# Performance work log

Hardware: AMD Instinct MI355X
Metric: run time of the kernel (lower is better)

Reference implementation:

```python
import jax, jax.numpy as jnp
import numpy as np

DIM = 256
DEPTH = 6
HEADS = 8
DH = DIM // HEADS            # 32
BUCKET = 64
TEMP = 0.75                  # sort-net softmax temperature
FF = 4 * DIM
B, T = 4, 8192


def layernorm(x, g, b, eps=1e-5):
    m = x.mean(-1, keepdims=True)
    v = ((x - m) ** 2).mean(-1, keepdims=True)
    return (x - m) * jax.lax.rsqrt(v + eps) * g + b


def sinkhorn_attn(q, k, v):
    # q,k,v: (bh, t, dh). Bucketed attention with differentiable top-1 bucket routing
    bh, t, dh = q.shape
    nb = t // BUCKET
    bq = q.reshape(bh, nb, BUCKET, dh)
    bk = k.reshape(bh, nb, BUCKET, dh)
    bv = v.reshape(bh, nb, BUCKET, dh)
    # sort net: bucket summaries -> routing matrix R (differentiable_topk, k=1)
    sq = bq.mean(2)                                   # (bh, nb, dh)
    sk = bk.mean(2)
    R = jnp.einsum('bie,bje->bij', sq, sk) * (dh ** -0.5)
    probs = jax.nn.softmax(R / TEMP, axis=-1)
    top = jnp.max(probs, axis=-1, keepdims=True)      # (bh, nb, 1)
    idx = jnp.argmax(probs, axis=-1)                  # (bh, nb)
    Rtop = jax.nn.one_hot(idx, nb, dtype=q.dtype) * top
    # gather routed key/value buckets (weighted by routing prob)
    bk_r = jnp.einsum('bij,bjtd->bitd', Rtop, bk)
    bv_r = jnp.einsum('bij,bjtd->bitd', Rtop, bv)
    K = jnp.concatenate([bk_r, bk], axis=2)           # (bh, nb, 2*BUCKET, dh)
    V = jnp.concatenate([bv_r, bv], axis=2)
    dots = jnp.einsum('buie,buje->buij', bq, K) * (dh ** -0.5)
    attn = jax.nn.softmax(dots, axis=-1)
    out = jnp.einsum('buij,buje->buie', attn, V)
    return out.reshape(bh, t, dh)


def setup_inputs() -> dict:
    key = jax.random.key(0)
    ks = jax.random.split(key, 18)
    s = 0.02
    f32 = jnp.float32
    inp = {
        'x': jax.random.normal(ks[0], (B, DIM, T), f32),
        'pe0': jax.random.normal(ks[1], (T // BUCKET, DIM), f32) * s,
        'pe1': jax.random.normal(ks[2], (BUCKET, DIM), f32) * s,
        'ln1_g': jnp.ones((DEPTH, DIM), f32),
        'ln1_b': jnp.zeros((DEPTH, DIM), f32),
        'Wq': jax.random.normal(ks[3], (DEPTH, DIM, DIM), f32) * s,
        'Wkv': jax.random.normal(ks[4], (DEPTH, DIM, 2 * DIM), f32) * s,
        'Wo': jax.random.normal(ks[5], (DEPTH, DIM, DIM), f32) * s,
        'bo': jnp.zeros((DEPTH, DIM), f32),
        'ln2_g': jnp.ones((DEPTH, DIM), f32),
        'ln2_b': jnp.zeros((DEPTH, DIM), f32),
        'W1': jax.random.normal(ks[6], (DEPTH, DIM, FF), f32) * s,
        'b1': jnp.zeros((DEPTH, FF), f32),
        'W2': jax.random.normal(ks[7], (DEPTH, FF, DIM), f32) * s,
        'b2': jnp.zeros((DEPTH, DIM), f32),
        'gf': jnp.ones((DIM,), f32),
        'bf': jnp.zeros((DIM,), f32),
    }
    return inp


def _forward(x, pe0, pe1, ln1_g, ln1_b, Wq, Wkv, Wo, bo, ln2_g, ln2_b, W1, b1, W2, b2, gf, bf):
    b, _, t = x.shape
    y = jnp.transpose(x, (0, 2, 1))                      # (b, t, dim)
    pos = (pe0[:, None, :] + pe1[None, :, :]).reshape(-1, DIM)[:t]
    y = y + pos

    def split_heads(u):
        return u.reshape(b, t, HEADS, DH).transpose(0, 2, 1, 3).reshape(b * HEADS, t, DH)

    def step(y, p):
        g1, b1_, wq, wkv, wo, bo_, g2, b2_, w1, bb1, w2, bb2 = p
        h = layernorm(y, g1, b1_)
        q = h @ wq
        k, v = jnp.split(h @ wkv, 2, axis=-1)
        o = sinkhorn_attn(split_heads(q), split_heads(k), split_heads(v))
        o = o.reshape(b, HEADS, t, DH).transpose(0, 2, 1, 3).reshape(b, t, DIM)
        y = y + o @ wo + bo_
        h = layernorm(y, g2, b2_)
        y = y + jax.nn.gelu(h @ w1 + bb1, approximate=False) @ w2 + bb2
        return y, None

    y, _ = jax.lax.scan(step, y, (ln1_g, ln1_b, Wq, Wkv, Wo, bo, ln2_g, ln2_b, W1, b1, W2, b2))
    y = layernorm(y, gf, bf)
    return jnp.transpose(y, (0, 2, 1))


def reference(x, pe0, pe1, ln1_g, ln1_b, Wq, Wkv, Wo, bo, ln2_g, ln2_b, W1, b1, W2, b2, gf, bf):
    return _forward(x, pe0, pe1, ln1_g, ln1_b, Wq, Wkv, Wo, bo, ln2_g, ln2_b, W1, b1, W2, b2, gf, bf)
```

## Files before the change

### kernel.cpp

```cpp
#include <hip/hip_runtime.h>
#include <cstdint>
#include <cstddef>

#define T_LEN 8192
#define DIMC  256
#define NBUCK 128
#define BHEAD 32
#define MROWS 32768

typedef __attribute__((ext_vector_type(8))) short bf16x8;
typedef __attribute__((ext_vector_type(4))) float f32x4;

__device__ __forceinline__ ushort f2bf(float x) {
  union { float f; unsigned u; } v; v.f = x;
  unsigned r = v.u + 0x7fffu + ((v.u >> 16) & 1u);
  return (ushort)(r >> 16);
}
__device__ __forceinline__ float bf2f(ushort u) {
  union { unsigned u; float f; } v; v.u = ((unsigned)u) << 16; return v.f;
}

__device__ __forceinline__ void gld16(const void* g, void* l) {
  __builtin_amdgcn_global_load_lds((const __attribute__((address_space(1))) void*)g,
                                   (__attribute__((address_space(3))) void*)l, 16, 0, 0);
}

__device__ __forceinline__ float fast_gelu(float v) {
  float t2 = fmaf(v * v, 0.07135481283f, 1.5957691216f);
  float z  = v * t2;
  float e  = __expf(-z);
  return v * __builtin_amdgcn_rcpf(1.0f + e);
}

__global__ __launch_bounds__(256)
void add_pos_k(const float* __restrict__ x, const float* __restrict__ pe0,
               const float* __restrict__ pe1, float* __restrict__ y) {
  __shared__ float tile[32][33];
  int b  = blockIdx.z;
  int t0 = blockIdx.x * 32;
  int d0 = blockIdx.y * 32;
  int tj = threadIdx.x;
  int di = threadIdx.y;
#pragma unroll
  for (int k = 0; k < 4; k++) {
    int d = d0 + di + k * 8;
    tile[di + k * 8][tj] = x[((size_t)b * DIMC + d) * T_LEN + t0 + tj];
  }
  __syncthreads();
#pragma unroll
  for (int k = 0; k < 4; k++) {
    int t = t0 + di + k * 8;
    int d = d0 + tj;
    y[((size_t)b * T_LEN + t) * DIMC + d] =
        tile[tj][di + k * 8] + pe0[(size_t)(t >> 6) * DIMC + d] + pe1[(size_t)(t & 63) * DIMC + d];
  }
}

__global__ __launch_bounds__(256)
void layernorm_k(const float* __restrict__ x, const float* __restrict__ g,
                 const float* __restrict__ b, ushort* __restrict__ o) {
  int row  = blockIdx.x * 4 + (threadIdx.x >> 6);
  int lane = threadIdx.x & 63;
  const float4* xr = (const float4*)(x + (size_t)row * DIMC);
  float4 v = xr[lane];
  float s  = v.x + v.y + v.z + v.w;
  float s2 = v.x * v.x + v.y * v.y + v.z * v.z + v.w * v.w;
#pragma unroll
  for (int off = 32; off; off >>= 1) {
    s  += __shfl_xor(s, off);
    s2 += __shfl_xor(s2, off);
  }
  float mean = s * (1.0f / 256.0f);
  float var  = s2 * (1.0f / 256.0f) - mean * mean;
  float r    = rsqrtf(var + 1e-5f);
  float4 gv = ((const float4*)g)[lane];
  float4 bv = ((const float4*)b)[lane];
  ushort4 o4;
  o4.x = f2bf((v.x - mean) * r * gv.x + bv.x);
  o4.y = f2bf((v.y - mean) * r * gv.y + bv.y);
  o4.z = f2bf((v.z - mean) * r * gv.z + bv.z);
  o4.w = f2bf((v.w - mean) * r * gv.w + bv.w);
  ((ushort4*)(o + (size_t)row * DIMC))[lane] = o4;
}

__global__ __launch_bounds__(256)
void wt_bf16_k(const float* __restrict__ W, ushort* __restrict__ Wt,
               int K, int N, size_t outStride) {
  __shared__ float t[32][33];
  int l = blockIdx.z;
  const float* Wl = W + (size_t)l * K * N;
  ushort* Wtl = Wt + (size_t)l * outStride;
  int n0 = blockIdx.x * 32, k0 = blockIdx.y * 32;
  int tx = threadIdx.x, ty = threadIdx.y;
#pragma unroll
  for (int p = 0; p < 4; p++)
    t[ty + p * 8][tx] = Wl[(size_t)(k0 + ty + p * 8) * N + n0 + tx];
  __syncthreads();
#pragma unroll
  for (int p = 0; p < 4; p++)
    Wtl[(size_t)(n0 + ty + p * 8) * K + k0 + tx] = f2bf(t[tx][ty + p * 8]);
}

template <int EPI>
__global__ __launch_bounds__(256)
void gemm_bf16(const ushort* __restrict__ A, const ushort* __restrict__ Bt,
               const float* __restrict__ bias, ushort* __restrict__ Cbf,
               int N, int K, int lda, int ldb) {
  __shared__ ushort As[128 * 32];
  __shared__ ushort Bs[128 * 32];
  __shared__ ushort eb[4][16][66];
  int tid = threadIdx.x;
  int w = tid >> 6, lane = tid & 63;
  int bm = blockIdx.x << 7, bn = blockIdx.y << 7;
  int wm = (w >> 1) << 6, wn = (w & 1) << 6;
  int l15 = lane & 15, quad = lane >> 4;

  int off0 = (w << 11) + (lane << 4);
  int off1 = off0 + 1024;
  int r0 = off0 >> 6;
  int r1 = off1 >> 6;
  int swc = (((lane & 3) ^ ((lane >> 3) & 3)) << 3);
  const ushort* ga0 = A + (size_t)(bm + r0) * lda + swc;
  const ushort* ga1 = A + (size_t)(bm + r1) * lda + swc;
  const ushort* gb0 = Bt + (size_t)(bn + r0) * ldb + swc;
  const ushort* gb1 = Bt + (size_t)(bn + r1) * ldb + swc;
  ushort* lA0 = As + (w << 10);
  ushort* lA1 = lA0 + 512;
  ushort* lB0 = Bs + (w << 10);
  ushort* lB1 = lB0 + 512;

  int sq = quad ^ ((l15 >> 1) & 3);

  f32x4 acc[4][4];
#pragma unroll
  for (int i = 0; i < 4; i++)
#pragma unroll
    for (int j = 0; j < 4; j++) {
      f32x4 z = {0.f, 0.f, 0.f, 0.f};
      acc[i][j] = z;
    }

  for (int k0 = 0; k0 < K; k0 += 32) {
    gld16(ga0 + k0, lA0);
    gld16(ga1 + k0, lA1);
    gld16(gb0 + k0, lB0);
    gld16(gb1 + k0, lB1);
    __syncthreads();
    bf16x8 aF[4], bF[4];
#pragma unroll
    for (int i = 0; i < 4; i++)
      aF[i] = *(const bf16x8*)(As + ((wm + (i << 4) + l15) << 5) + (sq << 3));
#pragma unroll
    for (int j = 0; j < 4; j++)
      bF[j] = *(const bf16x8*)(Bs + ((wn + (j << 4) + l15) << 5) + (sq << 3));
#pragma unroll
    for (int i = 0; i < 4; i++)
#pragma unroll
      for (int j = 0; j < 4; j++)
        acc[i][j] = __builtin_amdgcn_mfma_f32_16x16x32_bf16(aF[i], bF[j], acc[i][j], 0, 0, 0);
    __syncthreads();
  }

  float bvj[4];
  if (EPI == 1) {
#pragma unroll
    for (int j = 0; j < 4; j++) bvj[j] = bias[bn + wn + (j << 4) + l15];
  }
#pragma unroll
  for (int i = 0; i < 4; i++) {
#pragma unroll
    for (int j = 0; j < 4; j++) {
#pragma unroll
      for (int r = 0; r < 4; r++) {
        float v = acc[i][j][r];
        if (EPI == 1) v = fast_gelu(v + bvj[j]);
        eb[w][(quad << 2) + r][(j << 4) + l15] = f2bf(v);
      }
    }
#pragma unroll
    for (int h = 0; h < 2; h++) {
      int chunk = (h << 6) + lane;
      int row = chunk >> 3, c8 = (chunk & 7) << 3;
      bf16x8 vv = *(const bf16x8*)&eb[w][row][c8];
      *(bf16x8*)&Cbf[(size_t)(bm + wm + (i << 4) + row) * N + bn + wn + c8] = vv;
    }
  }
}

template <int FINAL>
__global__ __launch_bounds__(256)
void oproj_ln_k(const ushort* __restrict__ A, const ushort* __restrict__ Bt,
                const float* __restrict__ bias, float* __restrict__ y,
                const float* __restrict__ g, const float* __restrict__ b,
                ushort* __restrict__ obf, int K, int lda) {
  __shared__ ushort smem[64 * 264];
  __shared__ float red[2][64][2];
  __shared__ float stat[64][2];
  ushort* As = smem;
  ushort* Bs = smem + 2048;
  int tid = threadIdx.x;
  int wid = tid >> 6, lane = tid & 63;
  int l15 = lane & 15, quad = lane >> 4;
  int bm = blockIdx.x << 6;
  int wm = (wid >> 1) << 5;
  int wn = (wid & 1) << 7;

  int swc = (((tid & 3) ^ ((tid >> 3) & 3)) << 3);
  const ushort* gaA = A + (size_t)(bm + (tid >> 2)) * lda + swc;
  ushort* lA = As + (tid << 3);
  const ushort* gaB[4];
  ushort* lB[4];
#pragma unroll
  for (int p = 0; p < 4; p++) {
    int u = (p << 8) + tid;
    gaB[p] = Bt + (size_t)(u >> 2) * K + swc;
    lB[p] = Bs + (u << 3);
  }

  int sq = quad ^ ((l15 >> 1) & 3);

  f32x4 acc[2][8];
#pragma unroll
  for (int i = 0; i < 2; i++)
#pragma unroll
    for (int j = 0; j < 8; j++) {
      f32x4 z = {0.f, 0.f, 0.f, 0.f};
      acc[i][j] = z;
    }

  for (int k0 = 0; k0 < K; k0 += 32) {
    gld16(gaA + k0, lA);
#pragma unroll
    for (int p = 0; p < 4; p++) gld16(gaB[p] + k0, lB[p]);
    __syncthreads();
    bf16x8 aF[2];
#pragma unroll
    for (int i = 0; i < 2; i++)
      aF[i] = *(const bf16x8*)(As + ((wm + (i << 4) + l15) << 5) + (sq << 3));
#pragma unroll
    for (int j = 0; j < 8; j++) {
      bf16x8 bF = *(const bf16x8*)(Bs + ((wn + (j << 4) + l15) << 5) + (sq << 3));
#pragma unroll
      for (int i = 0; i < 2; i++)
        acc[i][j] = __builtin_amdgcn_mfma_f32_16x16x32_bf16(aF[i], bF, acc[i][j], 0, 0, 0);
    }
    __syncthreads();
  }

  float bc[8];
#pragma unroll
  for (int j = 0; j < 8; j++) bc[j] = bias[wn + (j << 4) + l15];
  float s1v[2][4], s2v[2][4];
#pragma unroll
  for (int i = 0; i < 2; i++)
#pragma unroll
    for (int r = 0; r < 4; r++) {
      int row = bm + wm + (i << 4) + (quad << 2) + r;
      float s1 = 0.f, s2 = 0.f;
#pragma unroll
      for (int j = 0; j < 8; j++) {
        size_t idx = (size_t)row * 256 + wn + (j << 4) + l15;
        float v = acc[i][j][r] + bc[j] + y[idx];
        acc[i][j][r] = v;
        if (!FINAL) y[idx] = v;
        s1 += v;
        s2 += v * v;
      }
      s1v[i][r] = s1;
      s2v[i][r] = s2;
    }
#pragma unroll
  for (int off = 1; off < 16; off <<= 1)
#pragma unroll
    for (int i = 0; i < 2; i++)
#pragma unroll
      for (int r = 0; r < 4; r++) {
        s1v[i][r] += __shfl_xor(s1v[i][r], off);
        s2v[i][r] += __shfl_xor(s2v[i][r], off);
      }
  if (l15 == 0) {
#pragma unroll
    for (int i = 0; i < 2; i++)
#pragma unroll
      for (int r = 0; r < 4; r++) {
        int lr = wm + (i << 4) + (quad << 2) + r;
        red[wid & 1][lr][0] = s1v[i][r];
        red[wid & 1][lr][1] = s2v[i][r];
      }
  }
  __syncthreads();
  if (tid < 64) {
    float s  = red[0][tid][0] + red[1][tid][0];
    float s2 = red[0][tid][1] + red[1][tid][1];
    float mean = s * (1.0f / 256.0f);
    float var  = s2 * (1.0f / 256.0f) - mean * mean;
    stat[tid][0] = mean;
    stat[tid][1] = rsqrtf(var + 1e-5f);
  }
  __syncthreads();

  if (FINAL) {
#pragma unroll
    for (int j = 0; j < 8; j++) {
      int col = wn + (j << 4) + l15;
      float gc = g[col], bc2 = b[col];
#pragma unroll
      for (int i = 0; i < 2; i++)
#pragma unroll
        for (int r = 0; r < 4; r++) {
          int lr = wm + (i << 4) + (quad << 2) + r;
          float o = (acc[i][j][r] - stat[lr][0]) * stat[lr][1] * gc + bc2;
          y[(size_t)(bm + lr) * 256 + col] = o;
        }
    }
  } else {
    ushort (*eb)[264] = (ushort(*)[264])smem;
#pragma unroll
    for (int j = 0; j < 8; j++) {
      int col = wn + (j << 4) + l15;
      float gc = g[col], bc2 = b[col];
#pragma unroll
      for (int i = 0; i < 2; i++)
#pragma unroll
        for (int r = 0; r < 4; r++) {
          int lr = wm + (i << 4) + (quad << 2) + r;
          float o = (acc[i][j][r] - stat[lr][0]) * stat[lr][1] * gc + bc2;
          eb[lr][col] = f2bf(o);
        }
    }
    __syncthreads();
#pragma unroll
    for (int h = 0; h < 8; h++) {
      int chunk = (h << 8) + tid;
      int row = chunk >> 5, c8 = (chunk & 31) << 3;
      bf16x8 vv = *(const bf16x8*)&eb[row][c8];
      *(bf16x8*)&obf[(size_t)(bm + row) * 256 + c8] = vv;
    }
  }
}

__global__ __launch_bounds__(64)
void summary_k(const ushort* __restrict__ qkv,
               float* __restrict__ sq, float* __restrict__ sk) {
  int blk = blockIdx.x;
  int bh = blk >> 7, ib = blk & 127;
  int b = bh >> 3, h = bh & 7;
  int lane = threadIdx.x;
  int d = lane & 31;
  bool isK = lane >= 32;
  size_t base = ((size_t)b * T_LEN + (size_t)ib * 64) * 768 + (isK ? 256 : 0) + h * 32 + d;
  float s = 0.f;
#pragma unroll 8
  for (int t = 0; t < 64; t++) s += bf2f(qkv[base + (size_t)t * 768]);
  s *= (1.0f / 64.0f);
  float* dst = isK ? sk : sq;
  dst[((size_t)bh * NBUCK + ib) * 32 + d] = s;
}

__global__ __launch_bounds__(64)
void route_k(const float* __restrict__ sq, const float* __restrict__ sk,
             int* __restrict__ ridx, float* __restrict__ rw) {
  int blk = blockIdx.x;
  int bh = blk >> 7, ib = blk & 127;
  int lane = threadIdx.x;
  const float* qrow = sq + ((size_t)bh * NBUCK + ib) * 32;
  const float* k0 = sk + ((size_t)bh * NBUCK + lane) * 32;
  const float* k1 = k0 + 64 * 32;
  float s0 = 0.f, s1 = 0.f;
#pragma unroll
  for (int d = 0; d < 32; d++) {
    float qd = qrow[d];
    s0 += qd * k0[d];
    s1 += qd * k1[d];
  }
  const float sc = 0.17677669529663687f * (4.0f / 3.0f);
  float L0 = s0 * sc, L1 = s1 * sc;
  float m = fmaxf(L0, L1);
#pragma unroll
  for (int off = 32; off; off >>= 1) m = fmaxf(m, __shfl_xor(m, off));
  float Z = expf(L0 - m) + expf(L1 - m);
#pragma unroll
  for (int off = 32; off; off >>= 1) Z += __shfl_xor(Z, off);
  float mv = (L1 > L0) ? L1 : L0;
  int mj = (L1 > L0) ? lane + 64 : lane;
#pragma unroll
  for (int off = 32; off; off >>= 1) {
    float ov = __shfl_xor(mv, off);
    int oj = __shfl_xor(mj, off);
    if (ov > mv || (ov == mv && oj < mj)) { mv = ov; mj = oj; }
  }
  if (lane == 0) {
    ridx[blk] = mj;
    rw[blk] = 1.0f / Z;
  }
}

__global__ __launch_bounds__(256)
void attn_mfma_k(const ushort* __restrict__ qkv,
                 const int* __restrict__ ridx, const float* __restrict__ rw,
                 ushort* __restrict__ o) {
  __shared__ ushort Qs[64][40];
  __shared__ ushort Ks[128][40];
  __shared__ ushort Vt[32][136];
  __shared__ ushort Ps[4][16][136];
  int blk = blockIdx.x;
  int bh = blk >> 7, ib = blk & 127;
  int b = bh >> 3, h = bh & 7;
  int tid = threadIdx.x;
  int jr = ridx[blk];
  float w = rw[blk];
  {
    int r = tid >> 2, c = (tid & 3) << 3;
    const ushort* src = qkv + ((size_t)b * T_LEN + (size_t)ib * 64 + r) * 768 + h * 32 + c;
    *(bf16x8*)&Qs[r][c] = *(const bf16x8*)src;
  }
#pragma unroll
  for (int p = 0; p < 2; p++) {
    int idx = tid + (p << 8);
    int r = idx >> 2, c = (idx & 3) << 3;
    int srcb = (r < 64) ? jr : ib;
    int tt = r & 63;
    const ushort* src = qkv + ((size_t)b * T_LEN + (size_t)srcb * 64 + tt) * 768 + 256 + h * 32 + c;
    *(bf16x8*)&Ks[r][c] = *(const bf16x8*)src;
  }
  {
    int tok = tid >> 1, d0 = (tid & 1) << 4;
    int srcb = (tok < 64) ? jr : ib;
    int tt = tok & 63;
    const ushort* src = qkv + ((size_t)b * T_LEN + (size_t)srcb * 64 + tt) * 768 + 512 + h * 32 + d0;
    bf16x8 v0 = *(const bf16x8*)src;
    bf16x8 v1 = *(const bf16x8*)(src + 8);
#pragma unroll
    for (int j = 0; j < 8; j++) {
      Vt[d0 + j][tok] = (ushort)v0[j];
      Vt[d0 + 8 + j][tok] = (ushort)v1[j];
    }
  }
  __syncthreads();
  int wid = tid >> 6, lane = tid & 63, l15 = lane & 15, quad = lane >> 4;
  bf16x8 aQ = *(const bf16x8*)&Qs[(wid << 4) + l15][quad << 3];
  f32x4 sf[8];
#pragma unroll
  for (int jn = 0; jn < 8; jn++) {
    bf16x8 bK = *(const bf16x8*)&Ks[(jn << 4) + l15][quad << 3];
    f32x4 z = {0.f, 0.f, 0.f, 0.f};
    sf[jn] = __builtin_amdgcn_mfma_f32_16x16x32_bf16(aQ, bK, z, 0, 0, 0);
  }
  const float sc = 0.17677669529663687f;
#pragma unroll
  for (int jn = 0; jn < 8; jn++) {
    float mult = (jn < 4) ? w * sc : sc;
#pragma unroll
    for (int r = 0; r < 4; r++) sf[jn][r] *= mult;
  }
  float mx[4], sm[4], inv[4];
#pragma unroll
  for (int r = 0; r < 4; r++) {
    float m = sf[0][r];
#pragma unroll
    for (int jn = 1; jn < 8; jn++) m = fmaxf(m, sf[jn][r]);
    mx[r] = m;
  }
#pragma unroll
  for (int off = 1; off < 16; off <<= 1)
#pragma unroll
    for (int r = 0; r < 4; r++) mx[r] = fmaxf(mx[r], __shfl_xor(mx[r], off));
#pragma unroll
  for (int r = 0; r < 4; r++) sm[r] = 0.f;
#pragma unroll
  for (int jn = 0; jn < 8; jn++)
#pragma unroll
    for (int r = 0; r < 4; r++) {
      sf[jn][r] = __expf(sf[jn][r] - mx[r]);
      sm[r] += sf[jn][r];
    }
#pragma unroll
  for (int off = 1; off < 16; off <<= 1)
#pragma unroll
    for (int r = 0; r < 4; r++) sm[r] += __shfl_xor(sm[r], off);
#pragma unroll
  for (int r = 0; r < 4; r++) inv[r] = __builtin_amdgcn_rcpf(sm[r]);
#pragma unroll
  for (int jn = 0; jn < 8; jn++) {
    float ws2 = (jn < 4) ? w : 1.f;
#pragma unroll
    for (int r = 0; r < 4; r++)
      Ps[wid][(quad << 2) + r][(jn << 4) + l15] = f2bf(sf[jn][r] * inv[r] * ws2);
  }
  f32x4 of[2];
#pragma unroll
  for (int nd = 0; nd < 2; nd++) { f32x4 z = {0.f, 0.f, 0.f, 0.f}; of[nd] = z; }
#pragma unroll
  for (int kk = 0; kk < 4; kk++) {
    bf16x8 aP = *(const bf16x8*)&Ps[wid][l15][(kk << 5) + (quad << 3)];
#pragma unroll
    for (int nd = 0; nd < 2; nd++) {
      bf16x8 bV = *(const bf16x8*)&Vt[(nd << 4) + l15][(kk << 5) + (quad << 3)];
      of[nd] = __builtin_amdgcn_mfma_f32_16x16x32_bf16(aP, bV, of[nd], 0, 0, 0);
    }
  }
  ushort* obase = o + ((size_t)b * T_LEN + (size_t)ib * 64 + (wid << 4) + (quad << 2)) * 256 + h * 32 + l15;
#pragma unroll
  for (int nd = 0; nd < 2; nd++)
#pragma unroll
    for (int r = 0; r < 4; r++)
      obase[(size_t)r * 256 + (nd << 4)] = f2bf(of[nd][r]);
}

__global__ __launch_bounds__(256)
void transpose_out_k(const float* __restrict__ yln, float* __restrict__ out) {
  __shared__ float tile[32][33];
  int b  = blockIdx.z;
  int t0 = blockIdx.x * 32;
  int d0 = blockIdx.y * 32;
  int tx = threadIdx.x;
  int ty = threadIdx.y;
#pragma unroll
  for (int k = 0; k < 4; k++) {
    int t = t0 + ty + k * 8;
    tile[ty + k * 8][tx] = yln[((size_t)b * T_LEN + t) * DIMC + d0 + tx];
  }
  __syncthreads();
#pragma unroll
  for (int k = 0; k < 4; k++) {
    int d = d0 + ty + k * 8;
    out[((size_t)b * DIMC + d) * T_LEN + t0 + tx] = tile[tx][ty + k * 8];
  }
}

extern "C" void kernel_launch(void* const* d_in, const int* in_sizes, int n_in,
                              void* d_out, int out_size, void* d_ws, size_t ws_size,
                              hipStream_t stream) {
  const float* x     = (const float*)d_in[0];
  const float* pe0   = (const float*)d_in[1];
  const float* pe1   = (const float*)d_in[2];
  const float* ln1_g = (const float*)d_in[3];
  const float* ln1_b = (const float*)d_in[4];
  const float* Wq    = (const float*)d_in[5];
  const float* Wkv   = (const float*)d_in[6];
  const float* Wo    = (const float*)d_in[7];
  const float* bo    = (const float*)d_in[8];
  const float* ln2_g = (const float*)d_in[9];
  const float* ln2_b = (const float*)d_in[10];
  const float* W1    = (const float*)d_in[11];
  const float* b1    = (const float*)d_in[12];
  const float* W2    = (const float*)d_in[13];
  const float* b2    = (const float*)d_in[14];
  const float* gf    = (const float*)d_in[15];
  const float* bfp   = (const float*)d_in[16];
  float* out = (float*)d_out;

  const int M = MROWS;
  float*  y    = (float*)d_ws;
  ushort* qkv  = (ushort*)(y + (size_t)M * 256);
  ushort* bufA = qkv + (size_t)M * 768;
  ushort* bufB = bufA + (size_t)M * 256;
  ushort* wbf  = bufB + (size_t)M * 256;
  float*  sqb  = (float*)(wbf + (size_t)6 * 786432);
  float*  skb  = sqb + 131072;
  float*  rwb  = skb + 131072;
  int*    rib  = (int*)(rwb + 4096);
  ushort* ffbf = qkv;

  dim3 tb(32, 8);
  wt_bf16_k<<<dim3(8, 8, 6),  tb, 0, stream>>>(Wq,  wbf + 0,      256, 256,  786432);
  wt_bf16_k<<<dim3(16, 8, 6), tb, 0, stream>>>(Wkv, wbf + 65536,  256, 512,  786432);
  wt_bf16_k<<<dim3(8, 8, 6),  tb, 0, stream>>>(Wo,  wbf + 196608, 256, 256,  786432);
  wt_bf16_k<<<dim3(32, 8, 6), tb, 0, stream>>>(W1,  wbf + 262144, 256, 1024, 786432);
  wt_bf16_k<<<dim3(8, 32, 6), tb, 0, stream>>>(W2,  wbf + 524288, 1024, 256, 786432);

  add_pos_k<<<dim3(T_LEN / 32, DIMC / 32, 4), tb, 0, stream>>>(x, pe0, pe1, y);
  layernorm_k<<<M / 4, 256, 0, stream>>>(y, ln1_g, ln1_b, bufB);

  for (int l = 0; l < 6; l++) {
    const ushort* wl    = wbf + (size_t)l * 786432;
    const ushort* wqkvT = wl;
    const ushort* woT   = wl + 196608;
    const ushort* w1T   = wl + 262144;
    const ushort* w2T   = wl + 524288;

    gemm_bf16<0><<<dim3(M / 128, 6), 256, 0, stream>>>(bufB, wqkvT, nullptr, qkv, 768, 256, 256, 256);
    summary_k<<<BHEAD * NBUCK, 64, 0, stream>>>(qkv, sqb, skb);
    route_k<<<BHEAD * NBUCK, 64, 0, stream>>>(sqb, skb, rib, rwb);
    attn_mfma_k<<<BHEAD * NBUCK, 256, 0, stream>>>(qkv, rib, rwb, bufA);
    oproj_ln_k<0><<<M / 64, 256, 0, stream>>>(bufA, woT, bo + l * 256, y,
                                              ln2_g + l * 256, ln2_b + l * 256,
                                              bufB, 256, 256);
    gemm_bf16<1><<<dim3(M / 128, 8), 256, 0, stream>>>(bufB, w1T, b1 + l * 1024, ffbf, 1024, 256, 256, 256);
    if (l < 5) {
      oproj_ln_k<0><<<M / 64, 256, 0, stream>>>(ffbf, w2T, b2 + l * 256, y,
                                                ln1_g + (l + 1) * 256, ln1_b + (l + 1) * 256,
                                                bufB, 1024, 1024);
    } else {
      oproj_ln_k<1><<<M / 64, 256, 0, stream>>>(ffbf, w2T, b2 + l * 256, y,
                                                gf, bfp, nullptr, 1024, 1024);
    }
  }

  transpose_out_k<<<dim3(T_LEN / 32, DIMC / 32, 4), tb, 0, stream>>>(y, out);

  (void)in_sizes; (void)n_in; (void)out_size; (void)ws_size;
}
```

Before: 1.167 ms.

## Double-buffer LDS tiles in bf16 GEMM and output-projection kernels

Both GEMM kernels now use two LDS buffers: the next K-slice is issued with global_load_lds before the MFMA work on the current slice, so global latency can hide behind compute, and one barrier per iteration is removed. The epilogue scratch in gemm_bf16 is aliased onto the first buffer. This raises LDS per block (gemm_bf16 to 32 KB, oproj to about 40 KB plus reductions), which could lower occupancy.

```diff
diff --git a/kernel.cpp b/kernel.cpp
--- a/kernel.cpp
+++ b/kernel.cpp
@@ -106,9 +106,7 @@
 void gemm_bf16(const ushort* __restrict__ A, const ushort* __restrict__ Bt,
                const float* __restrict__ bias, ushort* __restrict__ Cbf,
                int N, int K, int lda, int ldb) {
-  __shared__ ushort As[128 * 32];
-  __shared__ ushort Bs[128 * 32];
-  __shared__ ushort eb[4][16][66];
+  __shared__ ushort sm[2][8192];
   int tid = threadIdx.x;
   int w = tid >> 6, lane = tid & 63;
   int bm = blockIdx.x << 7, bn = blockIdx.y << 7;
@@ -116,18 +114,17 @@
   int l15 = lane & 15, quad = lane >> 4;
 
   int off0 = (w << 11) + (lane << 4);
-  int off1 = off0 + 1024;
   int r0 = off0 >> 6;
-  int r1 = off1 >> 6;
+  int r1 = (off0 + 1024) >> 6;
   int swc = (((lane & 3) ^ ((lane >> 3) & 3)) << 3);
   const ushort* ga0 = A + (size_t)(bm + r0) * lda + swc;
   const ushort* ga1 = A + (size_t)(bm + r1) * lda + swc;
   const ushort* gb0 = Bt + (size_t)(bn + r0) * ldb + swc;
   const ushort* gb1 = Bt + (size_t)(bn + r1) * ldb + swc;
-  ushort* lA0 = As + (w << 10);
-  ushort* lA1 = lA0 + 512;
-  ushort* lB0 = Bs + (w << 10);
-  ushort* lB1 = lB0 + 512;
+  int aoff0 = (w << 10) + 0;
+  int aoff1 = aoff0 + 512;
+  int boff0 = 4096 + (w << 10);
+  int boff1 = boff0 + 512;
 
   int sq = quad ^ ((l15 >> 1) & 3);
 
@@ -140,27 +137,39 @@
       acc[i][j] = z;
     }
 
+  gld16(ga0, &sm[0][aoff0]);
+  gld16(ga1, &sm[0][aoff1]);
+  gld16(gb0, &sm[0][boff0]);
+  gld16(gb1, &sm[0][boff1]);
+  __syncthreads();
+
+  int cur = 0;
   for (int k0 = 0; k0 < K; k0 += 32) {
-    gld16(ga0 + k0, lA0);
-    gld16(ga1 + k0, lA1);
-    gld16(gb0 + k0, lB0);
-    gld16(gb1 + k0, lB1);
-    __syncthreads();
+    if (k0 + 32 < K) {
+      ushort* S = sm[cur ^ 1];
+      gld16(ga0 + k0 + 32, S + aoff0);
+      gld16(ga1 + k0 + 32, S + aoff1);
+      gld16(gb0 + k0 + 32, S + boff0);
+      gld16(gb1 + k0 + 32, S + boff1);
+    }
+    const ushort* Sc = sm[cur];
     bf16x8 aF[4], bF[4];
 #pragma unroll
     for (int i = 0; i < 4; i++)
-      aF[i] = *(const bf16x8*)(As + ((wm + (i << 4) + l15) << 5) + (sq << 3));
+      aF[i] = *(const bf16x8*)(Sc + ((wm + (i << 4) + l15) << 5) + (sq << 3));
 #pragma unroll
     for (int j = 0; j < 4; j++)
-      bF[j] = *(const bf16x8*)(Bs + ((wn + (j << 4) + l15) << 5) + (sq << 3));
+      bF[j] = *(const bf16x8*)(Sc + 4096 + ((wn + (j << 4) + l15) << 5) + (sq << 3));
 #pragma unroll
     for (int i = 0; i < 4; i++)
 #pragma unroll
       for (int j = 0; j < 4; j++)
         acc[i][j] = __builtin_amdgcn_mfma_f32_16x16x32_bf16(aF[i], bF[j], acc[i][j], 0, 0, 0);
     __syncthreads();
-  }
-
+    cur ^= 1;
+  }
+
+  ushort (*eb)[16][66] = (ushort(*)[16][66])&sm[0][0];
   float bvj[4];
   if (EPI == 1) {
 #pragma unroll
@@ -193,11 +202,9 @@
                 const float* __restrict__ bias, float* __restrict__ y,
                 const float* __restrict__ g, const float* __restrict__ b,
                 ushort* __restrict__ obf, int K, int lda) {
-  __shared__ ushort smem[64 * 264];
+  __shared__ ushort smem[20480];
   __shared__ float red[2][64][2];
   __shared__ float stat[64][2];
-  ushort* As = smem;
-  ushort* Bs = smem + 2048;
   int tid = threadIdx.x;
   int wid = tid >> 6, lane = tid & 63;
   int l15 = lane & 15, quad = lane >> 4;
@@ -207,15 +214,16 @@
 
   int swc = (((tid & 3) ^ ((tid >> 3) & 3)) << 3);
   const ushort* gaA = A + (size_t)(bm + (tid >> 2)) * lda + swc;
-  ushort* lA = As + (tid << 3);
   const ushort* gaB[4];
-  ushort* lB[4];
 #pragma unroll
   for (int p = 0; p < 4; p++) {
     int u = (p << 8) + tid;
     gaB[p] = Bt + (size_t)(u >> 2) * K + swc;
-    lB[p] = Bs + (u << 3);
-  }
+  }
+  int lAoff = tid << 3;
+  int lBoff[4];
+#pragma unroll
+  for (int p = 0; p < 4; p++) lBoff[p] = 2048 + (((p << 8) + tid) << 3);
 
   int sq = quad ^ ((l15 >> 1) & 3);
 
@@ -228,23 +236,33 @@
       acc[i][j] = z;
     }
 
+  gld16(gaA, smem + lAoff);
+#pragma unroll
+  for (int p = 0; p < 4; p++) gld16(gaB[p], smem + lBoff[p]);
+  __syncthreads();
+
+  int cur = 0;
   for (int k0 = 0; k0 < K; k0 += 32) {
-    gld16(gaA + k0, lA);
-#pragma unroll
-    for (int p = 0; p < 4; p++) gld16(gaB[p] + k0, lB[p]);
-    __syncthreads();
+    if (k0 + 32 < K) {
+      ushort* S = smem + ((cur ^ 1) ? 10240 : 0);
+      gld16(gaA + k0 + 32, S + lAoff);
+#pragma unroll
+      for (int p = 0; p < 4; p++) gld16(gaB[p] + k0 + 32, S + lBoff[p]);
+    }
+    const ushort* Sc = smem + (cur ? 10240 : 0);
     bf16x8 aF[2];
 #pragma unroll
     for (int i = 0; i < 2; i++)
-      aF[i] = *(const bf16x8*)(As + ((wm + (i << 4) + l15) << 5) + (sq << 3));
+      aF[i] = *(const bf16x8*)(Sc + ((wm + (i << 4) + l15) << 5) + (sq << 3));
 #pragma unroll
     for (int j = 0; j < 8; j++) {
-      bf16x8 bF = *(const bf16x8*)(Bs + ((wn + (j << 4) + l15) << 5) + (sq << 3));
+      bf16x8 bF = *(const bf16x8*)(Sc + 2048 + ((wn + (j << 4) + l15) << 5) + (sq << 3));
 #pragma unroll
       for (int i = 0; i < 2; i++)
         acc[i][j] = __builtin_amdgcn_mfma_f32_16x16x32_bf16(aF[i], bF, acc[i][j], 0, 0, 0);
     }
     __syncthreads();
+    cur ^= 1;
   }
 
   float bc[8];
```

Result: faster. 1.124 ms (-3.7%).
